# Kernel optimization log

Hardware: AMD Instinct MI355X
Metric: run time of the kernel (lower is better)

The kernel has to match this reference:

```python
import jax, jax.numpy as jnp
import numpy as np
import math
from jax import lax

B, L = 64, 8192
S = L // 8          # width after 3 stride-(1,2) SAME convs
D = 4 * 5           # height(4) * channels(5) -> per-token feature dim
D_FLAT = S * D


def setup_inputs():
    key = jax.random.key(0)
    ks = jax.random.split(key, 32)
    sc = 0.1
    inp = {
        "inputs": jax.random.randint(ks[0], (B, L), 0, 4, dtype=jnp.int32),
        # conv stack: HWIO kernels, Conv2D(5,(4,4),(1,2),'SAME')
        "conv_w1": sc * jax.random.normal(ks[1], (4, 4, 1, 5), jnp.float32),
        "conv_b1": jnp.zeros((5,), jnp.float32),
        "conv_w2": sc * jax.random.normal(ks[2], (4, 4, 5, 5), jnp.float32),
        "conv_b2": jnp.zeros((5,), jnp.float32),
        "conv_w3": sc * jax.random.normal(ks[3], (4, 4, 5, 5), jnp.float32),
        "conv_b3": jnp.zeros((5,), jnp.float32),
        # 3 SelfAttn blocks, each with K/Q/V projections [D, D]
        "attn1_K": sc * jax.random.normal(ks[4], (D, D), jnp.float32),
        "attn1_Q": sc * jax.random.normal(ks[5], (D, D), jnp.float32),
        "attn1_V": sc * jax.random.normal(ks[6], (D, D), jnp.float32),
        "attn2_K": sc * jax.random.normal(ks[7], (D, D), jnp.float32),
        "attn2_Q": sc * jax.random.normal(ks[8], (D, D), jnp.float32),
        "attn2_V": sc * jax.random.normal(ks[9], (D, D), jnp.float32),
        "attn3_K": sc * jax.random.normal(ks[10], (D, D), jnp.float32),
        "attn3_Q": sc * jax.random.normal(ks[11], (D, D), jnp.float32),
        "attn3_V": sc * jax.random.normal(ks[12], (D, D), jnp.float32),
        # 3 Dense(10) layers (no activation, as in Keras defaults)
        "dense_w1": 0.01 * jax.random.normal(ks[13], (D_FLAT, 10), jnp.float32),
        "dense_b1": jnp.zeros((10,), jnp.float32),
        "dense_w2": sc * jax.random.normal(ks[14], (10, 10), jnp.float32),
        "dense_b2": jnp.zeros((10,), jnp.float32),
        "dense_w3": sc * jax.random.normal(ks[15], (10, 10), jnp.float32),
        "dense_b3": jnp.zeros((10,), jnp.float32),
    }
    return inp


def _conv(x, w, b):
    # NHWC, HWIO, strides (1,2), SAME
    y = lax.conv_general_dilated(x, w, window_strides=(1, 2), padding="SAME",
                                 dimension_numbers=("NHWC", "HWIO", "NHWC"))
    return y + b


def _self_attn(x, Kw, Qw, Vw):
    # x: [B, S, D]; manual causal scaled dot-product attention
    K = x @ Kw
    Q = x @ Qw
    V = x @ Vw
    s = Q.shape[1]
    mask = jnp.triu(jnp.full((s, s), -jnp.inf, dtype=x.dtype), k=1)
    scores = jnp.einsum("bsd,btd->bst", Q, K) / math.sqrt(K.shape[-1]) + mask
    return jax.nn.softmax(scores, axis=-1) @ V


def reference(inputs, conv_w1, conv_b1, conv_w2, conv_b2, conv_w3, conv_b3,
              attn1_K, attn1_Q, attn1_V, attn2_K, attn2_Q, attn2_V,
              attn3_K, attn3_Q, attn3_V,
              dense_w1, dense_b1, dense_w2, dense_b2, dense_w3, dense_b3):
    # one_hot over axis=1 -> [B, 4, L], then channel dim -> [B, 4, L, 1]
    x = jax.nn.one_hot(inputs, 4, axis=1, dtype=jnp.float32)[..., None]
    x = _conv(x, conv_w1, conv_b1)
    x = _conv(x, conv_w2, conv_b2)
    x = _conv(x, conv_w3, conv_b3)            # [B, 4, S, 5]
    # tokens along width, features = height(4) x channels(5)
    x = jnp.transpose(x, (0, 2, 1, 3)).reshape(x.shape[0], S, D)
    x = _self_attn(x, attn1_K, attn1_Q, attn1_V)
    x = _self_attn(x, attn2_K, attn2_Q, attn2_V)
    x = _self_attn(x, attn3_K, attn3_Q, attn3_V)
    x = x.reshape(x.shape[0], -1)             # flatten [B, S*D]
    x = x @ dense_w1 + dense_b1
    x = x @ dense_w2 + dense_b2
    x = x @ dense_w3 + dense_b3               # [B, 10]
    return x
```

## Files before the change

kernel.cpp:

```cpp
#include <hip/hip_runtime.h>
#include <hip/hip_bf16.h>


#define B_ 64
#define L_ 8192
#define S_ 1024
#define D_ 20

typedef unsigned short ushort_t;
typedef __attribute__((ext_vector_type(8))) short short8_t;
typedef __attribute__((ext_vector_type(4))) short short4_t;
typedef __attribute__((ext_vector_type(4))) float f32x4_t;

__device__ __forceinline__ ushort_t f2bf(float f) {
  unsigned u = __float_as_uint(f);
  return (ushort_t)((u + 0x7fffu + ((u >> 16) & 1u)) >> 16);
}
__device__ __forceinline__ float bf2f(ushort_t h) {
  return __uint_as_float(((unsigned)h) << 16);
}

__global__ __launch_bounds__(256) void conv12_kernel(
    const int* __restrict__ inp,
    const float* __restrict__ W1c, const float* __restrict__ B1c,
    const float* __restrict__ W2c, const float* __restrict__ B2c,
    float* __restrict__ out,
    const float* __restrict__ W1d,
    float* __restrict__ W1T) {
  __shared__ float w1s[80], b1s[5], w2s[400], b2s[5];
  for (int j = threadIdx.x; j < 400; j += 256) w2s[j] = W2c[j];
  if (threadIdx.x < 80)      w1s[threadIdx.x]      = W1c[threadIdx.x];
  else if (threadIdx.x < 85) b1s[threadIdx.x - 80] = B1c[threadIdx.x - 80];
  else if (threadIdx.x < 90) b2s[threadIdx.x - 85] = B2c[threadIdx.x - 85];
  __syncthreads();
  const int idx = blockIdx.x * 256 + threadIdx.x;
  const int b  = idx >> 11;
  const int wo = idx & 2047;
  const int* ib = inp + (size_t)b * L_;
  int iv[10];
#pragma unroll
  for (int t = 0; t < 10; ++t) {
    int g = 4 * wo - 3 + t;
    iv[t] = (g >= 0 && g < L_) ? ib[g] : -100;
  }
  float val[4][4][5];
#pragma unroll
  for (int pos = 0; pos < 4; ++pos) {
    const int w1 = 2 * wo - 1 + pos;
    const bool okp = (w1 >= 0 && w1 < 4096);
#pragma unroll
    for (int hi = 0; hi < 4; ++hi)
#pragma unroll
      for (int ci = 0; ci < 5; ++ci) val[hi][pos][ci] = okp ? b1s[ci] : 0.f;
    if (okp) {
#pragma unroll
      for (int kw = 0; kw < 4; ++kw) {
        const int gw = 2 * w1 - 1 + kw;
        if (gw >= 0 && gw < L_) {
          const int v = iv[2 * pos + kw];
#pragma unroll
          for (int hi = 0; hi < 4; ++hi) {
            const int kh = v - hi + 1;
            if (kh >= 0 && kh < 4) {
#pragma unroll
              for (int ci = 0; ci < 5; ++ci)
                val[hi][pos][ci] += w1s[(kh * 4 + kw) * 5 + ci];
            }
          }
        }
      }
    }
  }
  float acc[4][5];
#pragma unroll
  for (int h = 0; h < 4; ++h)
#pragma unroll
    for (int c = 0; c < 5; ++c) acc[h][c] = b2s[c];
#pragma unroll
  for (int kh = 0; kh < 4; ++kh)
#pragma unroll
    for (int kw = 0; kw < 4; ++kw)
#pragma unroll
      for (int ci = 0; ci < 5; ++ci) {
        const float* wp = w2s + ((kh * 4 + kw) * 5 + ci) * 5;
        float w0 = wp[0], w1v = wp[1], w2v = wp[2], w3 = wp[3], w4 = wp[4];
#pragma unroll
        for (int h = 0; h < 4; ++h) {
          int hi = h - 1 + kh;
          if (hi >= 0 && hi < 4) {
            float x = val[hi][kw][ci];
            acc[h][0] += w0 * x;  acc[h][1] += w1v * x; acc[h][2] += w2v * x;
            acc[h][3] += w3 * x;  acc[h][4] += w4 * x;
          }
        }
      }
  float* ob = out + (size_t)b * 4 * 2048 * 5;
#pragma unroll
  for (int h = 0; h < 4; ++h)
#pragma unroll
    for (int c = 0; c < 5; ++c) ob[(h * 2048 + wo) * 5 + c] = acc[h][c];
  for (int j = idx; j < 204800; j += 131072) {
    int col = j / 20480, i2 = j - col * 20480;
    W1T[j] = W1d[i2 * 10 + col];
  }
}

__global__ __launch_bounds__(256) void conv3_proj_kernel(
    const float* __restrict__ in,
    const float* __restrict__ W,  const float* __restrict__ Bi,
    const float* __restrict__ Kw, const float* __restrict__ Qw,
    const float* __restrict__ Vw,
    ushort_t* __restrict__ Qb, ushort_t* __restrict__ Kb,
    ushort_t* __restrict__ Vt) {
  constexpr int WIN = 2048;
  __shared__ float ws[400], bs[5];
  __shared__ float kw[400], qw[400], vw[400];
  for (int j = threadIdx.x; j < 400; j += 256) {
    ws[j] = W[j]; kw[j] = Kw[j]; qw[j] = Qw[j]; vw[j] = Vw[j];
  }
  if (threadIdx.x < 5) bs[threadIdx.x] = Bi[threadIdx.x];
  __syncthreads();
  const int r  = blockIdx.x * 256 + threadIdx.x;
  const int b  = r >> 10;
  const int wo = r & 1023;
  float val[4][4][5];
#pragma unroll
  for (int hi = 0; hi < 4; ++hi) {
    const float* ir = in + ((size_t)b * 4 + hi) * WIN * 5;
#pragma unroll
    for (int kwp = 0; kwp < 4; ++kwp) {
      int wi = 2 * wo - 1 + kwp;
      bool ok = (wi >= 0 && wi < WIN);
#pragma unroll
      for (int ci = 0; ci < 5; ++ci) val[hi][kwp][ci] = ok ? ir[wi * 5 + ci] : 0.f;
    }
  }
  float acc[4][5];
#pragma unroll
  for (int h = 0; h < 4; ++h)
#pragma unroll
    for (int c = 0; c < 5; ++c) acc[h][c] = bs[c];
#pragma unroll
  for (int kh = 0; kh < 4; ++kh)
#pragma unroll
    for (int kwp = 0; kwp < 4; ++kwp)
#pragma unroll
      for (int ci = 0; ci < 5; ++ci) {
        const float* wp = ws + ((kh * 4 + kwp) * 5 + ci) * 5;
        float w0 = wp[0], w1 = wp[1], w2 = wp[2], w3 = wp[3], w4 = wp[4];
#pragma unroll
        for (int h = 0; h < 4; ++h) {
          int hi = h - 1 + kh;
          if (hi >= 0 && hi < 4) {
            float x = val[hi][kwp][ci];
            acc[h][0] += w0 * x; acc[h][1] += w1 * x; acc[h][2] += w2 * x;
            acc[h][3] += w3 * x; acc[h][4] += w4 * x;
          }
        }
      }
  float x[D_];
#pragma unroll
  for (int h = 0; h < 4; ++h)
#pragma unroll
    for (int c = 0; c < 5; ++c) x[h * 5 + c] = acc[h][c];
  float q[D_], k[D_], v[D_];
#pragma unroll
  for (int j = 0; j < D_; ++j) { q[j] = 0.f; k[j] = 0.f; v[j] = 0.f; }
#pragma unroll
  for (int i = 0; i < D_; ++i) {
#pragma unroll
    for (int j = 0; j < D_; ++j) {
      q[j] += x[i] * qw[i * D_ + j];
      k[j] += x[i] * kw[i * D_ + j];
      v[j] += x[i] * vw[i * D_ + j];
    }
  }
  const float sc = 0.22360679774997896f;
  ushort_t qt[32], kt[32];
#pragma unroll
  for (int j = 0; j < D_; ++j) { qt[j] = f2bf(q[j] * sc); kt[j] = f2bf(k[j]); }
#pragma unroll
  for (int j = D_; j < 32; ++j) { qt[j] = 0; kt[j] = 0; }
  int4* qd = (int4*)(Qb + (size_t)r * 32);
  int4* kd = (int4*)(Kb + (size_t)r * 32);
#pragma unroll
  for (int j = 0; j < 4; ++j) {
    qd[j] = *(const int4*)(qt + 8 * j);
    kd[j] = *(const int4*)(kt + 8 * j);
  }
  ushort_t* vbase = Vt + ((size_t)b * 32) * 1024 + wo;
#pragma unroll
  for (int d = 0; d < D_; ++d) vbase[d * 1024] = f2bf(v[d]);
}

#define TT_ 128
template <bool FUSE>
__global__ __launch_bounds__(256) void attn_kernel(
    const ushort_t* __restrict__ Qb, const ushort_t* __restrict__ Kb,
    const ushort_t* __restrict__ Vt,
    const float* __restrict__ Kw2, const float* __restrict__ Qw2,
    const float* __restrict__ Vw2,
    ushort_t* __restrict__ Qb2, ushort_t* __restrict__ Kb2,
    ushort_t* __restrict__ Vt2,
    const float* __restrict__ W1T,
    float* __restrict__ part2) {
  const int b     = blockIdx.y;
  const int g     = (blockIdx.y >> 4) & 3;
  const int off   = 4 * (g >> 1);
  const int strip = (g & 1) ? ((15 - off - blockIdx.x) & 15)
                            : (((int)blockIdx.x + off) & 15);
  const int q0    = strip * 64;
  const int tid   = threadIdx.x;
  const int w     = tid >> 6;
  const int lane  = tid & 63;
  const int n     = lane & 15;
  const int quad  = lane >> 4;
  const int qbase = q0 + 16 * w;
  const int qg    = qbase + n;
  __shared__ ushort_t kts[128 * 40];
  __shared__ ushort_t vts[32 * 136];
  __shared__ float extraf[FUSE ? 2480 : 3840];
  if (FUSE) {
    float tmp[5];
#pragma unroll
    for (int u = 0; u < 5; ++u) {
      int j = tid + u * 256;
      if (j < 1200) {
        int m = j / 400, oo = j - m * 400;
        tmp[u] = (m == 0) ? Kw2[oo] : (m == 1) ? Qw2[oo] : Vw2[oo];
      }
    }
#pragma unroll
    for (int u = 0; u < 5; ++u) {
      int j = tid + u * 256;
      if (j < 1200) extraf[j] = tmp[u];
    }
  }
  const ushort_t* KbB = Kb + (size_t)b * 1024 * 32;
  const ushort_t* VtB = Vt + (size_t)b * 32 * 1024;
  short8_t qfrag = *(const short8_t*)(Qb + ((size_t)(b * 1024 + qbase + n)) * 32 + quad * 8);
  f32x4_t oA = {0.f, 0.f, 0.f, 0.f};
  f32x4_t oB = {0.f, 0.f, 0.f, 0.f};
  float lsum = 0.f;
  const f32x4_t zero = {0.f, 0.f, 0.f, 0.f};
  const int nt = q0 + 64;
  for (int t0 = 0; t0 < nt; t0 += TT_) {
    __syncthreads();
    for (int i = tid; i < 512; i += 256) {
      int row = i >> 2, qc = i & 3;
      *(int4*)(kts + row * 40 + qc * 8) =
          *(const int4*)(KbB + (size_t)(t0 + row) * 32 + qc * 8);
    }
    for (int i = tid; i < 320; i += 256) {
      int row = i >> 4, cc = i & 15;
      *(int4*)(vts + row * 136 + cc * 8) =
          *(const int4*)(VtB + (size_t)row * 1024 + t0 + cc * 8);
    }
    __syncthreads();
    short8_t kf[8];
#pragma unroll
    for (int hc = 0; hc < 8; ++hc)
      kf[hc] = *(const short8_t*)(kts + (hc * 16 + n) * 40 + quad * 8);
#pragma unroll
    for (int hc = 0; hc < 8; ++hc) {
      const int tg = t0 + hc * 16 + quad * 4;
      f32x4_t s = __builtin_amdgcn_mfma_f32_16x16x32_bf16(kf[hc], qfrag, zero, 0, 0, 0);
      ushort_t pk4[4];
#pragma unroll
      for (int r = 0; r < 4; ++r) {
        float p = (tg + r <= qg) ? __expf(s[r]) : 0.f;
        ushort_t h = f2bf(p);
        lsum += bf2f(h);
        pk4[r] = h;
      }
      short4_t pfrag = *(const short4_t*)pk4;
      short4_t vlo = *(const short4_t*)(vts + n * 136 + hc * 16 + quad * 4);
      short4_t vhi = *(const short4_t*)(vts + (16 + n) * 136 + hc * 16 + quad * 4);
      oA = __builtin_amdgcn_mfma_f32_16x16x16bf16_1k(vlo, pfrag, oA, 0, 0, 0);
      oB = __builtin_amdgcn_mfma_f32_16x16x16bf16_1k(vhi, pfrag, oB, 0, 0, 0);
    }
  }
  float l = lsum;
  l += __shfl_xor(l, 16, 64);
  l += __shfl_xor(l, 32, 64);
  const float inv = 1.f / l;
  if (FUSE) {
    float* pw  = extraf;
    float* oxw = extraf + 1200 + w * 320;
#pragma unroll
    for (int r = 0; r < 4; ++r) oxw[n * 20 + quad * 4 + r] = oA[r] * inv;
    if (quad == 0) {
#pragma unroll
      for (int r = 0; r < 4; ++r) oxw[n * 20 + 16 + r] = oB[r] * inv;
    }
    __asm__ volatile("s_waitcnt lgkmcnt(0)" ::: "memory");
    const int row  = lane >> 2;
    const int part = lane & 3;
    float x[D_];
#pragma unroll
    for (int i = 0; i < D_; ++i) x[i] = oxw[row * 20 + i];
    float qv[5], kv[5], vv[5];
#pragma unroll
    for (int jj = 0; jj < 5; ++jj) { qv[jj] = 0.f; kv[jj] = 0.f; vv[jj] = 0.f; }
#pragma unroll
    for (int i = 0; i < D_; ++i) {
      const float xi = x[i];
#pragma unroll
      for (int jj = 0; jj < 5; ++jj) {
        const int j = 5 * part + jj;
        kv[jj] += xi * pw[i * 20 + j];
        qv[jj] += xi * pw[400 + i * 20 + j];
        vv[jj] += xi * pw[800 + i * 20 + j];
      }
    }
    const float sc = 0.22360679774997896f;
    const int rg = b * 1024 + qbase + row;
    const int s  = rg & 1023;
#pragma unroll
    for (int jj = 0; jj < 5; ++jj) {
      const int j = 5 * part + jj;
      Kb2[(size_t)rg * 32 + j] = f2bf(kv[jj]);
      Qb2[(size_t)rg * 32 + j] = f2bf(qv[jj] * sc);
      Vt2[(size_t)b * 32768 + (size_t)j * 1024 + s] = f2bf(vv[jj]);
    }
    if (part == 0) {
#pragma unroll
      for (int u = 0; u < 6; ++u)
        *(unsigned*)(Kb2 + (size_t)rg * 32 + 20 + 2 * u) = 0u;
    } else if (part == 1) {
#pragma unroll
      for (int u = 0; u < 6; ++u)
        *(unsigned*)(Qb2 + (size_t)rg * 32 + 20 + 2 * u) = 0u;
    }
  } else {
    float* oxflat = extraf;
    float* oxw    = oxflat + w * 320;
    float* red    = extraf + 1280;
#pragma unroll
    for (int r = 0; r < 4; ++r) oxw[n * 20 + quad * 4 + r] = oA[r] * inv;
    if (quad == 0) {
#pragma unroll
      for (int r = 0; r < 4; ++r) oxw[n * 20 + 16 + r] = oB[r] * inv;
    }
    __syncthreads();
    float acc[10];
#pragma unroll
    for (int j = 0; j < 10; ++j) acc[j] = 0.f;
    const float* wb = W1T;
    const int base = q0 * 20;
#pragma unroll
    for (int k = 0; k < 5; ++k) {
      const int il = tid + 256 * k;
      const float xv = oxflat[il];
#pragma unroll
      for (int j = 0; j < 10; ++j)
        acc[j] += xv * wb[(size_t)j * 20480 + base + il];
    }
#pragma unroll
    for (int j = 0; j < 10; ++j) red[tid * 10 + j] = acc[j];
    __syncthreads();
    for (int off2 = 128; off2 > 0; off2 >>= 1) {
      if (tid < off2) {
#pragma unroll
        for (int j = 0; j < 10; ++j) red[tid * 10 + j] += red[(tid + off2) * 10 + j];
      }
      __syncthreads();
    }
    if (tid < 10) part2[((b << 4) + strip) * 10 + tid] = red[tid];
  }
}

__global__ __launch_bounds__(64) void dense_final(
    const float* __restrict__ part2,
    const float* __restrict__ B1,
    const float* __restrict__ W2, const float* __restrict__ B2,
    const float* __restrict__ W3, const float* __restrict__ B3,
    float* __restrict__ out) {
  const int b = blockIdx.x;
  __shared__ float y1[10], y2[10];
  if (threadIdx.x < 10) {
    int j = threadIdx.x;
    float s = 0.f;
#pragma unroll
    for (int st = 0; st < 16; ++st) s += part2[((b << 4) + st) * 10 + j];
    y1[j] = s + B1[j];
  }
  __syncthreads();
  if (threadIdx.x < 10) {
    int j = threadIdx.x;
    float s = B2[j];
#pragma unroll
    for (int i = 0; i < 10; ++i) s += y1[i] * W2[i * 10 + j];
    y2[j] = s;
  }
  __syncthreads();
  if (threadIdx.x < 10) {
    int j = threadIdx.x;
    float s = B3[j];
#pragma unroll
    for (int i = 0; i < 10; ++i) s += y2[i] * W3[i * 10 + j];
    out[b * 10 + j] = s;
  }
}

extern "C" void kernel_launch(void* const* d_in, const int* in_sizes, int n_in,
                              void* d_out, int out_size, void* d_ws, size_t ws_size,
                              hipStream_t stream) {
  const int*   inp = (const int*)d_in[0];
  const float* cw1 = (const float*)d_in[1];
  const float* cb1 = (const float*)d_in[2];
  const float* cw2 = (const float*)d_in[3];
  const float* cb2 = (const float*)d_in[4];
  const float* cw3 = (const float*)d_in[5];
  const float* cb3 = (const float*)d_in[6];
  const float* a1K = (const float*)d_in[7];
  const float* a1Q = (const float*)d_in[8];
  const float* a1V = (const float*)d_in[9];
  const float* a2K = (const float*)d_in[10];
  const float* a2Q = (const float*)d_in[11];
  const float* a2V = (const float*)d_in[12];
  const float* a3K = (const float*)d_in[13];
  const float* a3Q = (const float*)d_in[14];
  const float* a3V = (const float*)d_in[15];
  const float* dw1 = (const float*)d_in[16];
  const float* db1 = (const float*)d_in[17];
  const float* dw2 = (const float*)d_in[18];
  const float* db2 = (const float*)d_in[19];
  const float* dw3 = (const float*)d_in[20];
  const float* db3 = (const float*)d_in[21];
  float* outp = (float*)d_out;

  float* wsf = (float*)d_ws;
  ushort_t* qbA  = (ushort_t*)(wsf);
  ushort_t* kbA  = (ushort_t*)(wsf + 1048576);
  ushort_t* vtA  = (ushort_t*)(wsf + 2097152);
  float*    part2= wsf + 4456448;
  float*    w1t  = wsf + 4466688;
  ushort_t* qbB  = (ushort_t*)(wsf + 4671488);
  ushort_t* kbB  = (ushort_t*)(wsf + 5712384);
  ushort_t* vtB  = (ushort_t*)(wsf + 6760960);
  float*    c2   = wsf + 5242880;

  conv12_kernel<<<512, 256, 0, stream>>>(inp, cw1, cb1, cw2, cb2, c2, dw1, w1t);

  conv3_proj_kernel<<<256, 256, 0, stream>>>(c2, cw3, cb3, a1K, a1Q, a1V, qbA, kbA, vtA);
  attn_kernel<true><<<dim3(16, 64), 256, 0, stream>>>(
      qbA, kbA, vtA, a2K, a2Q, a2V, qbB, kbB, vtB, nullptr, nullptr);
  attn_kernel<true><<<dim3(16, 64), 256, 0, stream>>>(
      qbB, kbB, vtB, a3K, a3Q, a3V, qbA, kbA, vtA, nullptr, nullptr);
  attn_kernel<false><<<dim3(16, 64), 256, 0, stream>>>(
      qbA, kbA, vtA, nullptr, nullptr, nullptr, nullptr, nullptr, nullptr,
      w1t, part2);

  dense_final<<<64, 64, 0, stream>>>(part2, db1, dw2, db2, dw3, db3, outp);
}
```

Measured before the change: 216.3 us.

## Fuse conv1/conv2 into conv3+projection kernel, recomputing conv2 outputs per thread

Merges the conv1+conv2 kernel into the conv3+QKV projection kernel. Each thread now recomputes the four conv2 positions it needs straight from the raw token inputs instead of reading a stored intermediate. This removes one kernel launch and the global write and read of the conv2 activation buffer. In exchange, conv2 work is roughly doubled because neighbouring threads overlap, register pressure rises, and the grid shrinks from 512 to 256 blocks.

```diff
diff --git a/kernel.cpp b/kernel.cpp
--- a/kernel.cpp
+++ b/kernel.cpp
@@ -20,139 +20,127 @@
   return __uint_as_float(((unsigned)h) << 16);
 }
 
-__global__ __launch_bounds__(256) void conv12_kernel(
+__global__ __launch_bounds__(256) void conv123_proj_kernel(
     const int* __restrict__ inp,
     const float* __restrict__ W1c, const float* __restrict__ B1c,
     const float* __restrict__ W2c, const float* __restrict__ B2c,
-    float* __restrict__ out,
+    const float* __restrict__ W3c, const float* __restrict__ B3c,
+    const float* __restrict__ Kw, const float* __restrict__ Qw,
+    const float* __restrict__ Vw,
+    ushort_t* __restrict__ Qb, ushort_t* __restrict__ Kb,
+    ushort_t* __restrict__ Vt,
     const float* __restrict__ W1d,
     float* __restrict__ W1T) {
-  __shared__ float w1s[80], b1s[5], w2s[400], b2s[5];
-  for (int j = threadIdx.x; j < 400; j += 256) w2s[j] = W2c[j];
+  __shared__ float w1s[80], b1s[5], b2s[5], b3s[5];
+  __shared__ float w2s[400], w3s[400];
+  __shared__ float kw[400], qw[400], vw[400];
+  for (int j = threadIdx.x; j < 400; j += 256) {
+    w2s[j] = W2c[j]; w3s[j] = W3c[j];
+    kw[j] = Kw[j]; qw[j] = Qw[j]; vw[j] = Vw[j];
+  }
   if (threadIdx.x < 80)      w1s[threadIdx.x]      = W1c[threadIdx.x];
   else if (threadIdx.x < 85) b1s[threadIdx.x - 80] = B1c[threadIdx.x - 80];
   else if (threadIdx.x < 90) b2s[threadIdx.x - 85] = B2c[threadIdx.x - 85];
-  __syncthreads();
-  const int idx = blockIdx.x * 256 + threadIdx.x;
-  const int b  = idx >> 11;
-  const int wo = idx & 2047;
-  const int* ib = inp + (size_t)b * L_;
-  int iv[10];
-#pragma unroll
-  for (int t = 0; t < 10; ++t) {
-    int g = 4 * wo - 3 + t;
-    iv[t] = (g >= 0 && g < L_) ? ib[g] : -100;
-  }
-  float val[4][4][5];
-#pragma unroll
-  for (int pos = 0; pos < 4; ++pos) {
-    const int w1 = 2 * wo - 1 + pos;
-    const bool okp = (w1 >= 0 && w1 < 4096);
-#pragma unroll
-    for (int hi = 0; hi < 4; ++hi)
-#pragma unroll
-      for (int ci = 0; ci < 5; ++ci) val[hi][pos][ci] = okp ? b1s[ci] : 0.f;
-    if (okp) {
-#pragma unroll
-      for (int kw = 0; kw < 4; ++kw) {
-        const int gw = 2 * w1 - 1 + kw;
-        if (gw >= 0 && gw < L_) {
-          const int v = iv[2 * pos + kw];
-#pragma unroll
-          for (int hi = 0; hi < 4; ++hi) {
-            const int kh = v - hi + 1;
-            if (kh >= 0 && kh < 4) {
-#pragma unroll
-              for (int ci = 0; ci < 5; ++ci)
-                val[hi][pos][ci] += w1s[(kh * 4 + kw) * 5 + ci];
-            }
-          }
-        }
-      }
-    }
-  }
-  float acc[4][5];
-#pragma unroll
-  for (int h = 0; h < 4; ++h)
-#pragma unroll
-    for (int c = 0; c < 5; ++c) acc[h][c] = b2s[c];
-#pragma unroll
-  for (int kh = 0; kh < 4; ++kh)
-#pragma unroll
-    for (int kw = 0; kw < 4; ++kw)
-#pragma unroll
-      for (int ci = 0; ci < 5; ++ci) {
-        const float* wp = w2s + ((kh * 4 + kw) * 5 + ci) * 5;
-        float w0 = wp[0], w1v = wp[1], w2v = wp[2], w3 = wp[3], w4 = wp[4];
-#pragma unroll
-        for (int h = 0; h < 4; ++h) {
-          int hi = h - 1 + kh;
-          if (hi >= 0 && hi < 4) {
-            float x = val[hi][kw][ci];
-            acc[h][0] += w0 * x;  acc[h][1] += w1v * x; acc[h][2] += w2v * x;
-            acc[h][3] += w3 * x;  acc[h][4] += w4 * x;
-          }
-        }
-      }
-  float* ob = out + (size_t)b * 4 * 2048 * 5;
-#pragma unroll
-  for (int h = 0; h < 4; ++h)
-#pragma unroll
-    for (int c = 0; c < 5; ++c) ob[(h * 2048 + wo) * 5 + c] = acc[h][c];
-  for (int j = idx; j < 204800; j += 131072) {
-    int col = j / 20480, i2 = j - col * 20480;
-    W1T[j] = W1d[i2 * 10 + col];
-  }
-}
-
-__global__ __launch_bounds__(256) void conv3_proj_kernel(
-    const float* __restrict__ in,
-    const float* __restrict__ W,  const float* __restrict__ Bi,
-    const float* __restrict__ Kw, const float* __restrict__ Qw,
-    const float* __restrict__ Vw,
-    ushort_t* __restrict__ Qb, ushort_t* __restrict__ Kb,
-    ushort_t* __restrict__ Vt) {
-  constexpr int WIN = 2048;
-  __shared__ float ws[400], bs[5];
-  __shared__ float kw[400], qw[400], vw[400];
-  for (int j = threadIdx.x; j < 400; j += 256) {
-    ws[j] = W[j]; kw[j] = Kw[j]; qw[j] = Qw[j]; vw[j] = Vw[j];
-  }
-  if (threadIdx.x < 5) bs[threadIdx.x] = Bi[threadIdx.x];
+  else if (threadIdx.x < 95) b3s[threadIdx.x - 90] = B3c[threadIdx.x - 90];
   __syncthreads();
   const int r  = blockIdx.x * 256 + threadIdx.x;
   const int b  = r >> 10;
   const int wo = r & 1023;
-  float val[4][4][5];
-#pragma unroll
-  for (int hi = 0; hi < 4; ++hi) {
-    const float* ir = in + ((size_t)b * 4 + hi) * WIN * 5;
-#pragma unroll
-    for (int kwp = 0; kwp < 4; ++kwp) {
-      int wi = 2 * wo - 1 + kwp;
-      bool ok = (wi >= 0 && wi < WIN);
-#pragma unroll
-      for (int ci = 0; ci < 5; ++ci) val[hi][kwp][ci] = ok ? ir[wi * 5 + ci] : 0.f;
+  const int* ib = inp + (size_t)b * L_;
+  const int g0 = 8 * wo - 7;
+  int iv[22];
+#pragma unroll
+  for (int t = 0; t < 22; ++t) {
+    int g = g0 + t;
+    iv[t] = (g >= 0 && g < L_) ? ib[g] : -100;
+  }
+  float val3[4][4][5];
+#pragma unroll
+  for (int pos = 0; pos < 4; ++pos) {
+    const int p2 = 2 * wo - 1 + pos;
+    const bool ok2 = (p2 >= 0 && p2 < 2048);
+    if (!ok2) {
+#pragma unroll
+      for (int h = 0; h < 4; ++h)
+#pragma unroll
+        for (int c = 0; c < 5; ++c) val3[h][pos][c] = 0.f;
+    } else {
+      float v1[4][4][5];
+#pragma unroll
+      for (int kw2 = 0; kw2 < 4; ++kw2) {
+        const int p1 = 2 * p2 - 1 + kw2;
+        const bool ok1 = (p1 >= 0 && p1 < 4096);
+#pragma unroll
+        for (int hi = 0; hi < 4; ++hi)
+#pragma unroll
+          for (int ci = 0; ci < 5; ++ci) v1[hi][kw2][ci] = ok1 ? b1s[ci] : 0.f;
+        if (ok1) {
+#pragma unroll
+          for (int kw1 = 0; kw1 < 4; ++kw1) {
+            const int gw = 2 * p1 - 1 + kw1;
+            if (gw >= 0 && gw < L_) {
+              const int v = iv[4 * pos + 2 * kw2 + kw1];
+#pragma unroll
+              for (int hi = 0; hi < 4; ++hi) {
+                const int kh = v - hi + 1;
+                if (kh >= 0 && kh < 4) {
+#pragma unroll
+                  for (int ci = 0; ci < 5; ++ci)
+                    v1[hi][kw2][ci] += w1s[(kh * 4 + kw1) * 5 + ci];
+                }
+              }
+            }
+          }
+        }
+      }
+      float acc2[4][5];
+#pragma unroll
+      for (int h = 0; h < 4; ++h)
+#pragma unroll
+        for (int c = 0; c < 5; ++c) acc2[h][c] = b2s[c];
+#pragma unroll
+      for (int kh = 0; kh < 4; ++kh)
+#pragma unroll
+        for (int kw2 = 0; kw2 < 4; ++kw2)
+#pragma unroll
+          for (int ci = 0; ci < 5; ++ci) {
+            const float* wp = w2s + ((kh * 4 + kw2) * 5 + ci) * 5;
+            float w0 = wp[0], w1v = wp[1], w2v = wp[2], w3v = wp[3], w4v = wp[4];
+#pragma unroll
+            for (int h = 0; h < 4; ++h) {
+              int hi = h - 1 + kh;
+              if (hi >= 0 && hi < 4) {
+                float x = v1[hi][kw2][ci];
+                acc2[h][0] += w0 * x;  acc2[h][1] += w1v * x;
+                acc2[h][2] += w2v * x; acc2[h][3] += w3v * x;
+                acc2[h][4] += w4v * x;
+              }
+            }
+          }
+#pragma unroll
+      for (int h = 0; h < 4; ++h)
+#pragma unroll
+        for (int c = 0; c < 5; ++c) val3[h][pos][c] = acc2[h][c];
     }
   }
   float acc[4][5];
 #pragma unroll
   for (int h = 0; h < 4; ++h)
 #pragma unroll
-    for (int c = 0; c < 5; ++c) acc[h][c] = bs[c];
+    for (int c = 0; c < 5; ++c) acc[h][c] = b3s[c];
 #pragma unroll
   for (int kh = 0; kh < 4; ++kh)
 #pragma unroll
     for (int kwp = 0; kwp < 4; ++kwp)
 #pragma unroll
       for (int ci = 0; ci < 5; ++ci) {
-        const float* wp = ws + ((kh * 4 + kwp) * 5 + ci) * 5;
+        const float* wp = w3s + ((kh * 4 + kwp) * 5 + ci) * 5;
         float w0 = wp[0], w1 = wp[1], w2 = wp[2], w3 = wp[3], w4 = wp[4];
 #pragma unroll
         for (int h = 0; h < 4; ++h) {
           int hi = h - 1 + kh;
           if (hi >= 0 && hi < 4) {
-            float x = val[hi][kwp][ci];
+            float x = val3[hi][kwp][ci];
             acc[h][0] += w0 * x; acc[h][1] += w1 * x; acc[h][2] += w2 * x;
             acc[h][3] += w3 * x; acc[h][4] += w4 * x;
           }
@@ -191,6 +179,10 @@
   ushort_t* vbase = Vt + ((size_t)b * 32) * 1024 + wo;
 #pragma unroll
   for (int d = 0; d < D_; ++d) vbase[d * 1024] = f2bf(v[d]);
+  for (int j = r; j < 204800; j += 65536) {
+    int col = j / 20480, i2 = j - col * 20480;
+    W1T[j] = W1d[i2 * 10 + col];
+  }
 }
 
 #define TT_ 128
@@ -439,11 +431,9 @@
   ushort_t* qbB  = (ushort_t*)(wsf + 4671488);
   ushort_t* kbB  = (ushort_t*)(wsf + 5712384);
   ushort_t* vtB  = (ushort_t*)(wsf + 6760960);
-  float*    c2   = wsf + 5242880;
-
-  conv12_kernel<<<512, 256, 0, stream>>>(inp, cw1, cb1, cw2, cb2, c2, dw1, w1t);
-
-  conv3_proj_kernel<<<256, 256, 0, stream>>>(c2, cw3, cb3, a1K, a1Q, a1V, qbA, kbA, vtA);
+
+  conv123_proj_kernel<<<256, 256, 0, stream>>>(
+      inp, cw1, cb1, cw2, cb2, cw3, cb3, a1K, a1Q, a1V, qbA, kbA, vtA, dw1, w1t);
   attn_kernel<true><<<dim3(16, 64), 256, 0, stream>>>(
       qbA, kbA, vtA, a2K, a2Q, a2V, qbB, kbB, vtB, nullptr, nullptr);
   attn_kernel<true><<<dim3(16, 64), 256, 0, stream>>>(
```

New measurement: 358.4 us. +65.7%, slower.
